# Kernel optimization log

Measured on AMD Instinct MI355X. Metric: run time of the kernel, lower is better.

Reference implementation:

```python
import jax, jax.numpy as jnp
import numpy as np
from jax import lax

N = 4096
IN_DIM, HID, OUT_DIM = 8, 64, 4
N_CONV = 10


def setup_inputs() -> dict:
    key = jax.random.key(0)
    ks = jax.random.split(key, 16)
    s = 0.05
    inp = {
        "inputs": jax.random.normal(ks[0], (N, IN_DIM), jnp.float32),
        "emb_w": jax.random.normal(ks[1], (IN_DIM, HID), jnp.float32) * s,
        "emb_b": jnp.zeros((HID,), jnp.float32),
        "q_w": jax.random.normal(ks[2], (HID, HID), jnp.float32) * s,
        "q_b": jnp.zeros((HID,), jnp.float32),
        "k_w": jax.random.normal(ks[3], (HID, HID), jnp.float32) * s,
        "k_b": jnp.zeros((HID,), jnp.float32),
        # 10 asymmetric conv layers: 1x3 kernel, 3x1 kernel, PReLU scalar (torch default 0.25)
        "conv_w1": jax.random.normal(ks[4], (N_CONV, 3), jnp.float32) * 0.3,
        "conv_w2": jax.random.normal(ks[5], (N_CONV, 3), jnp.float32) * 0.3,
        "conv_a": jnp.full((N_CONV,), 0.25, jnp.float32),
        "gcn_w": jax.random.normal(ks[6], (OUT_DIM, HID), jnp.float32) * s,
        "gcn_b": jnp.zeros((HID,), jnp.float32),
        "gcn_a": jnp.float32(0.25),
        "mlp_w1": jax.random.normal(ks[7], (HID, HID // 2), jnp.float32) * s,
        "mlp_b1": jnp.zeros((HID // 2,), jnp.float32),
        "mlp_w2": jax.random.normal(ks[8], (HID // 2, OUT_DIM), jnp.float32) * s,
        "mlp_b2": jnp.zeros((OUT_DIM,), jnp.float32),
    }
    return inp


def _asym_layer(x, w1, w2, a):
    # x: [1,1,N,N]; w1 -> 1x3 conv, w2 -> 3x1 conv, a -> PReLU scalar
    k1 = w1.reshape(1, 1, 1, 3)
    k2 = w2.reshape(1, 1, 3, 1)
    dn = ("NCHW", "OIHW", "NCHW")
    o = (lax.conv_general_dilated(x, k1, (1, 1), [(0, 0), (1, 1)], dimension_numbers=dn)
         + lax.conv_general_dilated(x, k2, (1, 1), [(1, 1), (0, 0)], dimension_numbers=dn))
    return jnp.where(o >= 0, o, a * o)


def reference(inputs, emb_w, emb_b, q_w, q_b, k_w, k_b,
              conv_w1, conv_w2, conv_a,
              gcn_w, gcn_b, gcn_a, mlp_w1, mlp_b1, mlp_w2, mlp_b2):
    o = inputs[:, 4:]                                   # [N, 4]
    x = inputs @ emb_w + emb_b                          # [N, H]
    q = x @ q_w + q_b                                   # [N, D]
    k = x @ k_w + k_b                                   # [N, D]
    scores = (q @ k.T) / jnp.sqrt(jnp.float32(k.shape[-1]))
    attn = jax.nn.softmax(scores, axis=-1)              # [N, N]

    h = attn[None, None]                                # [1,1,N,N]
    for i in range(N_CONV):
        h = _asym_layer(h, conv_w1[i], conv_w2[i], conv_a[i])
    conv_features = h[0, 0]                             # [N, N]

    mask = (jax.nn.sigmoid(conv_features) > 0.5).astype(attn.dtype)
    adjacency = mask * attn                             # [N, N]
    calc = adjacency @ o                                # [N, 4]

    g = calc @ gcn_w + gcn_b
    g = jnp.where(g >= 0, g, gcn_a * g)                 # PReLU
    m = jnp.maximum(g @ mlp_w1 + mlp_b1, 0.0)
    return m @ mlp_w2 + mlp_b2                          # [N, 4]
```

## Files before the change

### kernel.cpp

```cpp
#include <hip/hip_runtime.h>
#include <hip/hip_fp16.h>

#define NROWS 4096
#define HID 64

typedef _Float16 f16x8 __attribute__((ext_vector_type(8)));
typedef float f32x4 __attribute__((ext_vector_type(4)));

static __device__ __forceinline__ __half2 u2h(unsigned u) {
  __half2 h; __builtin_memcpy(&h, &u, 4); return h;
}
static __device__ __forceinline__ unsigned h2u(__half2 h) {
  unsigned u; __builtin_memcpy(&u, &h, 4); return u;
}

__global__ __launch_bounds__(64) void k_embed(
    const float* __restrict__ inp, const float* __restrict__ emb_w,
    const float* __restrict__ emb_b, const float* __restrict__ q_w,
    const float* __restrict__ q_b, const float* __restrict__ k_w,
    const float* __restrict__ k_b, __half* __restrict__ qh,
    __half* __restrict__ kh, float* __restrict__ opk) {
  int row = blockIdx.x;
  int t = threadIdx.x;
  __shared__ float in_s[8];
  __shared__ float x_s[64];
  if (t < 8) in_s[t] = inp[row * 8 + t];
  __syncthreads();
  float acc = emb_b[t];
#pragma unroll
  for (int i = 0; i < 8; ++i) acc += in_s[i] * emb_w[i * 64 + t];
  x_s[t] = acc;
  __syncthreads();
  float qa = q_b[t], ka = k_b[t];
#pragma unroll
  for (int i = 0; i < 64; ++i) {
    float xv = x_s[i];
    qa += xv * q_w[i * 64 + t];
    ka += xv * k_w[i * 64 + t];
  }
  qh[row * 64 + t] = __float2half(qa * 0.125f);
  kh[row * 64 + t] = __float2half(ka);
  if (t < 4) opk[row * 4 + t] = inp[row * 8 + 4 + t];
}

__global__ __launch_bounds__(512, 2) void k_scores(
    const __half* __restrict__ qh, const __half* __restrict__ kh,
    float* __restrict__ S) {
  __shared__ float redm[8][16];
  __shared__ float reds[8][16];
  int t = threadIdx.x;
  int w = t >> 6;
  int l = t & 63;
  int m16 = l & 15;
  int g4 = l >> 4;
  int rb = blockIdx.x * 16;
  const uint4* qq = (const uint4*)qh;
  const uint4* kk = (const uint4*)kh;
  int qrow = rb + m16;
  f16x8 a0 = __builtin_bit_cast(f16x8, qq[qrow * 8 + g4]);
  f16x8 a1 = __builtin_bit_cast(f16x8, qq[qrow * 8 + 4 + g4]);
  f32x4 acc[32];
#pragma unroll
  for (int i = 0; i < 32; ++i) acc[i] = (f32x4){0.f, 0.f, 0.f, 0.f};
#pragma unroll
  for (int i = 0; i < 32; ++i) {
    int kcol = (w * 32 + i) * 16 + m16;
    f16x8 b0 = __builtin_bit_cast(f16x8, kk[kcol * 8 + g4]);
    f16x8 b1 = __builtin_bit_cast(f16x8, kk[kcol * 8 + 4 + g4]);
    acc[i] = __builtin_amdgcn_mfma_f32_16x16x32_f16(a0, b0, acc[i], 0, 0, 0);
    acc[i] = __builtin_amdgcn_mfma_f32_16x16x32_f16(a1, b1, acc[i], 0, 0, 0);
  }
  float m4[4] = {-1e30f, -1e30f, -1e30f, -1e30f};
#pragma unroll
  for (int i = 0; i < 32; ++i) {
#pragma unroll
    for (int c = 0; c < 4; ++c) m4[c] = fmaxf(m4[c], acc[i][c]);
  }
#pragma unroll
  for (int off = 1; off < 16; off <<= 1) {
#pragma unroll
    for (int c = 0; c < 4; ++c) m4[c] = fmaxf(m4[c], __shfl_xor(m4[c], off, 64));
  }
  if (m16 == 0) {
#pragma unroll
    for (int c = 0; c < 4; ++c) redm[w][g4 * 4 + c] = m4[c];
  }
  __syncthreads();
#pragma unroll
  for (int c = 0; c < 4; ++c) {
    float mm = redm[0][g4 * 4 + c];
#pragma unroll
    for (int ww = 1; ww < 8; ++ww) mm = fmaxf(mm, redm[ww][g4 * 4 + c]);
    m4[c] = mm;
  }
  float s4[4] = {0.f, 0.f, 0.f, 0.f};
#pragma unroll
  for (int i = 0; i < 32; ++i) {
#pragma unroll
    for (int c = 0; c < 4; ++c) {
      float e = __expf(acc[i][c] - m4[c]);
      acc[i][c] = e;
      s4[c] += e;
    }
  }
#pragma unroll
  for (int off = 1; off < 16; off <<= 1) {
#pragma unroll
    for (int c = 0; c < 4; ++c) s4[c] += __shfl_xor(s4[c], off, 64);
  }
  if (m16 == 0) {
#pragma unroll
    for (int c = 0; c < 4; ++c) reds[w][g4 * 4 + c] = s4[c];
  }
  __syncthreads();
  float li[4];
#pragma unroll
  for (int c = 0; c < 4; ++c) {
    float ss = reds[0][g4 * 4 + c];
#pragma unroll
    for (int ww = 1; ww < 8; ++ww) ss += reds[ww][g4 * 4 + c];
    li[c] = 1.0f / ss;
  }
#pragma unroll
  for (int i = 0; i < 32; ++i) {
    int col = (w * 32 + i) * 16 + m16;
#pragma unroll
    for (int c = 0; c < 4; ++c) {
      S[(size_t)(rb + g4 * 4 + c) * NROWS + col] = acc[i][c] * li[c];
    }
  }
}

#define SWH 128
#define SHH 50
#define SSTRH 130
#define OWW 236
#define OHH 30
#define GX 18
#define GY 137

__global__ __launch_bounds__(512, 2) void k_conv3(
    const float* __restrict__ attn, float* __restrict__ partial,
    const float* __restrict__ w1p, const float* __restrict__ w2p,
    const float* __restrict__ ap, const float* __restrict__ opk) {
  __shared__ unsigned buf[2][SHH * SSTRH];
  int tid = threadIdx.x;
  int bx = blockIdx.x, by = blockIdx.y;
  int gi0 = by * OHH - 10;
  int gj0 = bx * OWW - 10;
  bool edge = (bx == 0) || (bx == GX - 1) || (by == 0) || (by == GY - 1);
  if (!edge) {
    for (int idx = tid; idx < SHH * SWH; idx += 512) {
      int r = idx >> 7, d = idx & 127;
      float2 v = *(const float2*)(attn + (size_t)(gi0 + r) * NROWS + gj0 + 2 * d);
      buf[0][r * SSTRH + d] =
          h2u(__float22half2_rn(make_float2(v.x * 256.f, v.y * 256.f)));
    }
  } else {
    for (int idx = tid; idx < SHH * SWH; idx += 512) {
      int r = idx >> 7, d = idx & 127;
      int gi = gi0 + r, gj = gj0 + 2 * d;
      float a = 0.f, b = 0.f;
      if ((unsigned)gi < (unsigned)NROWS) {
        if ((unsigned)gj < (unsigned)NROWS) a = attn[(size_t)gi * NROWS + gj] * 256.f;
        if ((unsigned)(gj + 1) < (unsigned)NROWS) b = attn[(size_t)gi * NROWS + gj + 1] * 256.f;
      }
      buf[0][r * SSTRH + d] = h2u(__float22half2_rn(make_float2(a, b)));
    }
  }
  __syncthreads();

  int wv = tid >> 6, l = tid & 63;
  int rb = 1 + 6 * wv;
  int doff = 2 * l;
  __half2 CM0 = __float2half2_rn(1.f), CM1 = __float2half2_rn(1.f);
  if (edge) {
    float m0 = ((unsigned)(gj0 + 4 * l + 0) < (unsigned)NROWS) ? 1.f : 0.f;
    float m1 = ((unsigned)(gj0 + 4 * l + 1) < (unsigned)NROWS) ? 1.f : 0.f;
    float m2 = ((unsigned)(gj0 + 4 * l + 2) < (unsigned)NROWS) ? 1.f : 0.f;
    float m3 = ((unsigned)(gj0 + 4 * l + 3) < (unsigned)NROWS) ? 1.f : 0.f;
    CM0 = __float22half2_rn(make_float2(m0, m1));
    CM1 = __float22half2_rn(make_float2(m2, m3));
  }

  for (int p = 0; p < 10; ++p) {
    unsigned* src = buf[p & 1];
    unsigned* dst = buf[(p + 1) & 1];
    __half2 W10 = __float2half2_rn(w1p[3 * p]);
    __half2 W12 = __float2half2_rn(w1p[3 * p + 2]);
    __half2 WC  = __float2half2_rn(w1p[3 * p + 1] + w2p[3 * p + 1]);
    __half2 W20 = __float2half2_rn(w2p[3 * p]);
    __half2 W22 = __float2half2_rn(w2p[3 * p + 2]);
    __half2 AL  = __float2half2_rn(ap[p]);
    uint2 Vm = *(uint2*)&src[(rb - 1) * SSTRH + doff];
    uint2 Vc = *(uint2*)&src[rb * SSTRH + doff];
#pragma unroll
    for (int s = 0; s < 6; ++s) {
      int r = rb + s;
      uint2 Vp = *(uint2*)&src[(r + 1) * SSTRH + doff];
      unsigned Lm1 = (unsigned)__builtin_amdgcn_update_dpp(
          0, (int)Vc.y, 0x138, 0xF, 0xF, true);
      unsigned Hp1 = (unsigned)__builtin_amdgcn_update_dpp(
          0, (int)Vc.x, 0x130, 0xF, 0xF, true);
      unsigned SL0 = __builtin_amdgcn_alignbit(Vc.x, Lm1, 16);
      unsigned SR0 = __builtin_amdgcn_alignbit(Vc.y, Vc.x, 16);
      unsigned SR1 = __builtin_amdgcn_alignbit(Hp1, Vc.y, 16);
      __half2 o0 = __hmul2(WC, u2h(Vc.x));
      o0 = __hfma2(W10, u2h(SL0), o0);
      o0 = __hfma2(W12, u2h(SR0), o0);
      o0 = __hfma2(W20, u2h(Vm.x), o0);
      o0 = __hfma2(W22, u2h(Vp.x), o0);
      __half2 o1 = __hmul2(WC, u2h(Vc.y));
      o1 = __hfma2(W10, u2h(SR0), o1);
      o1 = __hfma2(W12, u2h(SR1), o1);
      o1 = __hfma2(W20, u2h(Vm.y), o1);
      o1 = __hfma2(W22, u2h(Vp.y), o1);
      {
        unsigned u0 = h2u(o0), ua0 = h2u(__hmul2(AL, o0)), r0;
        asm("v_pk_max_f16 %0, %1, %2" : "=v"(r0) : "v"(u0), "v"(ua0));
        o0 = u2h(r0);
        unsigned u1 = h2u(o1), ua1 = h2u(__hmul2(AL, o1)), r1;
        asm("v_pk_max_f16 %0, %1, %2" : "=v"(r1) : "v"(u1), "v"(ua1));
        o1 = u2h(r1);
      }
      if (edge) {
        o0 = __hmul2(o0, CM0);
        o1 = __hmul2(o1, CM1);
        if ((unsigned)(gi0 + r) >= (unsigned)NROWS) {
          o0 = __float2half2_rn(0.f);
          o1 = __float2half2_rn(0.f);
        }
      }
      uint2 res = {h2u(o0), h2u(o1)};
      *(uint2*)&dst[r * SSTRH + doff] = res;
      Vm = Vc; Vc = Vp;
    }
    __syncthreads();
  }

  const unsigned* fin = buf[0];
  int i = tid >> 4;
  int part = tid & 15;
  int gi = gi0 + 10 + i;
  float a0 = 0.f, a1 = 0.f, a2 = 0.f, a3 = 0.f;
  if (i < OHH && gi < NROWS) {
    for (int g = part; g < 59; g += 16) {
      int jc = 10 + 4 * g;
      int gj = gj0 + jc;
      if (gj + 3 < NROWS) {
        unsigned d0 = fin[(10 + i) * SSTRH + (jc >> 1)];
        unsigned d1 = fin[(10 + i) * SSTRH + (jc >> 1) + 1];
        __half2 h0 = u2h(d0), h1 = u2h(d1);
        float4 av = *(const float4*)(attn + (size_t)gi * NROWS + gj);
        const float4* op = (const float4*)opk;
        if (__low2float(h0) > 0.f)  { float4 o = op[gj + 0]; a0 += av.x * o.x; a1 += av.x * o.y; a2 += av.x * o.z; a3 += av.x * o.w; }
        if (__high2float(h0) > 0.f) { float4 o = op[gj + 1]; a0 += av.y * o.x; a1 += av.y * o.y; a2 += av.y * o.z; a3 += av.y * o.w; }
        if (__low2float(h1) > 0.f)  { float4 o = op[gj + 2]; a0 += av.z * o.x; a1 += av.z * o.y; a2 += av.z * o.z; a3 += av.z * o.w; }
        if (__high2float(h1) > 0.f) { float4 o = op[gj + 3]; a0 += av.w * o.x; a1 += av.w * o.y; a2 += av.w * o.z; a3 += av.w * o.w; }
      }
    }
  }
#pragma unroll
  for (int off = 1; off < 16; off <<= 1) {
    a0 += __shfl_xor(a0, off, 64);
    a1 += __shfl_xor(a1, off, 64);
    a2 += __shfl_xor(a2, off, 64);
    a3 += __shfl_xor(a3, off, 64);
  }
  if (part == 0 && i < OHH && gi < NROWS) {
    float4 r = {a0, a1, a2, a3};
    *(float4*)&partial[((size_t)bx * NROWS + gi) * 4] = r;
  }
}

__global__ __launch_bounds__(64) void k_head(
    const float* __restrict__ partial, const float* __restrict__ gcn_w,
    const float* __restrict__ gcn_b, const float* __restrict__ gcn_a,
    const float* __restrict__ w1, const float* __restrict__ b1,
    const float* __restrict__ w2, const float* __restrict__ b2,
    float* __restrict__ out) {
  int row = blockIdx.x;
  int t = threadIdx.x;
  __shared__ float c4[4];
  __shared__ float gs[64];
  __shared__ float ms[32];
  {
    int c = t & 3, gg = t >> 2;
    float s = partial[((size_t)gg * NROWS + row) * 4 + c];
    if (gg < GX - 16)
      s += partial[((size_t)(gg + 16) * NROWS + row) * 4 + c];
#pragma unroll
    for (int off = 4; off < 64; off <<= 1) s += __shfl_xor(s, off, 64);
    if (t < 4) c4[t] = s;
  }
  __syncthreads();
  float g = gcn_b[t];
#pragma unroll
  for (int d = 0; d < 4; ++d) g += c4[d] * gcn_w[d * 64 + t];
  float ga = gcn_a[0];
  gs[t] = (g >= 0.f) ? g : ga * g;
  __syncthreads();
  if (t < 32) {
    float mm = b1[t];
#pragma unroll
    for (int i = 0; i < 64; ++i) mm += gs[i] * w1[i * 32 + t];
    ms[t] = fmaxf(mm, 0.f);
  }
  __syncthreads();
  if (t < 4) {
    float o = b2[t];
#pragma unroll
    for (int i = 0; i < 32; ++i) o += ms[i] * w2[i * 4 + t];
    out[row * 4 + t] = o;
  }
}

extern "C" void kernel_launch(void* const* d_in, const int* in_sizes, int n_in,
                              void* d_out, int out_size, void* d_ws, size_t ws_size,
                              hipStream_t stream) {
  (void)in_sizes; (void)n_in; (void)out_size; (void)ws_size;
  const float* inp    = (const float*)d_in[0];
  const float* emb_w  = (const float*)d_in[1];
  const float* emb_b  = (const float*)d_in[2];
  const float* q_w    = (const float*)d_in[3];
  const float* q_b    = (const float*)d_in[4];
  const float* k_w    = (const float*)d_in[5];
  const float* k_b    = (const float*)d_in[6];
  const float* conv_w1 = (const float*)d_in[7];
  const float* conv_w2 = (const float*)d_in[8];
  const float* conv_a  = (const float*)d_in[9];
  const float* gcn_w  = (const float*)d_in[10];
  const float* gcn_b  = (const float*)d_in[11];
  const float* gcn_a  = (const float*)d_in[12];
  const float* mlp_w1 = (const float*)d_in[13];
  const float* mlp_b1 = (const float*)d_in[14];
  const float* mlp_w2 = (const float*)d_in[15];
  const float* mlp_b2 = (const float*)d_in[16];
  float* out = (float*)d_out;

  const size_t NN = (size_t)NROWS * NROWS;
  float* A       = (float*)d_ws;
  float* partial = A + NN;
  float* qhf     = partial + (size_t)GX * NROWS * 4;
  float* khf     = qhf + (size_t)NROWS * HID / 2;
  float* opk     = khf + (size_t)NROWS * HID / 2;

  k_embed<<<NROWS, 64, 0, stream>>>(inp, emb_w, emb_b, q_w, q_b, k_w, k_b,
                                    (__half*)qhf, (__half*)khf, opk);
  k_scores<<<NROWS / 16, 512, 0, stream>>>((const __half*)qhf,
                                           (const __half*)khf, A);
  k_conv3<<<dim3(GX, GY), 512, 0, stream>>>(A, partial, conv_w1, conv_w2,
                                            conv_a, opk);
  k_head<<<NROWS, 64, 0, stream>>>(partial, gcn_w, gcn_b, gcn_a, mlp_w1, mlp_b1,
                                   mlp_w2, mlp_b2, out);
}
```

Baseline: 129.0 us.

## Use larger single-buffered conv tiles with 4 half2 per lane in-place update

The fused 10-layer stencil kernel now uses a single LDS buffer updated in place instead of ping-pong buffers. Each wave handles 7 rows, keeping the first and last rows in registers until after a barrier so neighbouring waves still read old values. Tiles grow to 512 columns by 58 rows, cutting the 10-cell halo recompute overhead and the grid count (9x108). Each lane now processes 8 columns via uint4 loads, which raises register pressure and adds a second barrier per layer.

```diff
diff --git a/kernel.cpp b/kernel.cpp
--- a/kernel.cpp
+++ b/kernel.cpp
@@ -131,90 +131,101 @@
   }
 }
 
-#define SWH 128
-#define SHH 50
-#define SSTRH 130
-#define OWW 236
-#define OHH 30
-#define GX 18
-#define GY 137
-
-__global__ __launch_bounds__(512, 2) void k_conv3(
+#define CSD 256
+#define CSH 58
+#define COW 492
+#define COH 38
+#define CGX 9
+#define CGY 108
+
+__global__ __launch_bounds__(512, 2) void k_conv4(
     const float* __restrict__ attn, float* __restrict__ partial,
     const float* __restrict__ w1p, const float* __restrict__ w2p,
     const float* __restrict__ ap, const float* __restrict__ opk) {
-  __shared__ unsigned buf[2][SHH * SSTRH];
+  __shared__ unsigned buf[CSH * CSD];
   int tid = threadIdx.x;
   int bx = blockIdx.x, by = blockIdx.y;
-  int gi0 = by * OHH - 10;
-  int gj0 = bx * OWW - 10;
-  bool edge = (bx == 0) || (bx == GX - 1) || (by == 0) || (by == GY - 1);
+  int gi0 = by * COH - 10;
+  int gj0 = bx * COW - 10;
+  bool edge = (bx == 0) || (bx == CGX - 1) || (by == 0) || (by == CGY - 1);
   if (!edge) {
-    for (int idx = tid; idx < SHH * SWH; idx += 512) {
-      int r = idx >> 7, d = idx & 127;
+    for (int idx = tid; idx < CSH * CSD; idx += 512) {
+      int r = idx >> 8, d = idx & 255;
       float2 v = *(const float2*)(attn + (size_t)(gi0 + r) * NROWS + gj0 + 2 * d);
-      buf[0][r * SSTRH + d] =
-          h2u(__float22half2_rn(make_float2(v.x * 256.f, v.y * 256.f)));
+      buf[idx] = h2u(__float22half2_rn(make_float2(v.x * 256.f, v.y * 256.f)));
     }
   } else {
-    for (int idx = tid; idx < SHH * SWH; idx += 512) {
-      int r = idx >> 7, d = idx & 127;
+    for (int idx = tid; idx < CSH * CSD; idx += 512) {
+      int r = idx >> 8, d = idx & 255;
       int gi = gi0 + r, gj = gj0 + 2 * d;
       float a = 0.f, b = 0.f;
       if ((unsigned)gi < (unsigned)NROWS) {
         if ((unsigned)gj < (unsigned)NROWS) a = attn[(size_t)gi * NROWS + gj] * 256.f;
         if ((unsigned)(gj + 1) < (unsigned)NROWS) b = attn[(size_t)gi * NROWS + gj + 1] * 256.f;
       }
-      buf[0][r * SSTRH + d] = h2u(__float22half2_rn(make_float2(a, b)));
+      buf[idx] = h2u(__float22half2_rn(make_float2(a, b)));
     }
   }
   __syncthreads();
 
   int wv = tid >> 6, l = tid & 63;
-  int rb = 1 + 6 * wv;
-  int doff = 2 * l;
-  __half2 CM0 = __float2half2_rn(1.f), CM1 = __float2half2_rn(1.f);
+  int rb = 1 + 7 * wv;
+  int doff = 4 * l;
+  __half2 CM[4];
+#pragma unroll
+  for (int d = 0; d < 4; ++d) CM[d] = __float2half2_rn(1.f);
   if (edge) {
-    float m0 = ((unsigned)(gj0 + 4 * l + 0) < (unsigned)NROWS) ? 1.f : 0.f;
-    float m1 = ((unsigned)(gj0 + 4 * l + 1) < (unsigned)NROWS) ? 1.f : 0.f;
-    float m2 = ((unsigned)(gj0 + 4 * l + 2) < (unsigned)NROWS) ? 1.f : 0.f;
-    float m3 = ((unsigned)(gj0 + 4 * l + 3) < (unsigned)NROWS) ? 1.f : 0.f;
-    CM0 = __float22half2_rn(make_float2(m0, m1));
-    CM1 = __float22half2_rn(make_float2(m2, m3));
+#pragma unroll
+    for (int d = 0; d < 4; ++d) {
+      float mlo = ((unsigned)(gj0 + 8 * l + 2 * d) < (unsigned)NROWS) ? 1.f : 0.f;
+      float mhi = ((unsigned)(gj0 + 8 * l + 2 * d + 1) < (unsigned)NROWS) ? 1.f : 0.f;
+      CM[d] = __float22half2_rn(make_float2(mlo, mhi));
+    }
   }
 
   for (int p = 0; p < 10; ++p) {
-    unsigned* src = buf[p & 1];
-    unsigned* dst = buf[(p + 1) & 1];
     __half2 W10 = __float2half2_rn(w1p[3 * p]);
     __half2 W12 = __float2half2_rn(w1p[3 * p + 2]);
     __half2 WC  = __float2half2_rn(w1p[3 * p + 1] + w2p[3 * p + 1]);
     __half2 W20 = __float2half2_rn(w2p[3 * p]);
     __half2 W22 = __float2half2_rn(w2p[3 * p + 2]);
     __half2 AL  = __float2half2_rn(ap[p]);
-    uint2 Vm = *(uint2*)&src[(rb - 1) * SSTRH + doff];
-    uint2 Vc = *(uint2*)&src[rb * SSTRH + doff];
-#pragma unroll
-    for (int s = 0; s < 6; ++s) {
+    uint4 Vm = *(uint4*)&buf[(rb - 1) * CSD + doff];
+    uint4 Vc = *(uint4*)&buf[rb * CSD + doff];
+    uint4 dfirst, dlast;
+#pragma unroll
+    for (int s = 0; s < 7; ++s) {
       int r = rb + s;
-      uint2 Vp = *(uint2*)&src[(r + 1) * SSTRH + doff];
+      uint4 Vp = *(uint4*)&buf[(r + 1) * CSD + doff];
       unsigned Lm1 = (unsigned)__builtin_amdgcn_update_dpp(
-          0, (int)Vc.y, 0x138, 0xF, 0xF, true);
+          0, (int)Vc.w, 0x138, 0xF, 0xF, true);
       unsigned Hp1 = (unsigned)__builtin_amdgcn_update_dpp(
           0, (int)Vc.x, 0x130, 0xF, 0xF, true);
-      unsigned SL0 = __builtin_amdgcn_alignbit(Vc.x, Lm1, 16);
-      unsigned SR0 = __builtin_amdgcn_alignbit(Vc.y, Vc.x, 16);
-      unsigned SR1 = __builtin_amdgcn_alignbit(Hp1, Vc.y, 16);
+      unsigned A0 = __builtin_amdgcn_alignbit(Vc.x, Lm1, 16);
+      unsigned A1 = __builtin_amdgcn_alignbit(Vc.y, Vc.x, 16);
+      unsigned A2 = __builtin_amdgcn_alignbit(Vc.z, Vc.y, 16);
+      unsigned A3 = __builtin_amdgcn_alignbit(Vc.w, Vc.z, 16);
+      unsigned A4 = __builtin_amdgcn_alignbit(Hp1, Vc.w, 16);
       __half2 o0 = __hmul2(WC, u2h(Vc.x));
-      o0 = __hfma2(W10, u2h(SL0), o0);
-      o0 = __hfma2(W12, u2h(SR0), o0);
+      o0 = __hfma2(W10, u2h(A0), o0);
+      o0 = __hfma2(W12, u2h(A1), o0);
       o0 = __hfma2(W20, u2h(Vm.x), o0);
       o0 = __hfma2(W22, u2h(Vp.x), o0);
       __half2 o1 = __hmul2(WC, u2h(Vc.y));
-      o1 = __hfma2(W10, u2h(SR0), o1);
-      o1 = __hfma2(W12, u2h(SR1), o1);
+      o1 = __hfma2(W10, u2h(A1), o1);
+      o1 = __hfma2(W12, u2h(A2), o1);
       o1 = __hfma2(W20, u2h(Vm.y), o1);
       o1 = __hfma2(W22, u2h(Vp.y), o1);
+      __half2 o2 = __hmul2(WC, u2h(Vc.z));
+      o2 = __hfma2(W10, u2h(A2), o2);
+      o2 = __hfma2(W12, u2h(A3), o2);
+      o2 = __hfma2(W20, u2h(Vm.z), o2);
+      o2 = __hfma2(W22, u2h(Vp.z), o2);
+      __half2 o3 = __hmul2(WC, u2h(Vc.w));
+      o3 = __hfma2(W10, u2h(A3), o3);
+      o3 = __hfma2(W12, u2h(A4), o3);
+      o3 = __hfma2(W20, u2h(Vm.w), o3);
+      o3 = __hfma2(W22, u2h(Vp.w), o3);
       {
         unsigned u0 = h2u(o0), ua0 = h2u(__hmul2(AL, o0)), r0;
         asm("v_pk_max_f16 %0, %1, %2" : "=v"(r0) : "v"(u0), "v"(ua0));
@@ -222,37 +233,50 @@
         unsigned u1 = h2u(o1), ua1 = h2u(__hmul2(AL, o1)), r1;
         asm("v_pk_max_f16 %0, %1, %2" : "=v"(r1) : "v"(u1), "v"(ua1));
         o1 = u2h(r1);
+        unsigned u2 = h2u(o2), ua2 = h2u(__hmul2(AL, o2)), r2;
+        asm("v_pk_max_f16 %0, %1, %2" : "=v"(r2) : "v"(u2), "v"(ua2));
+        o2 = u2h(r2);
+        unsigned u3 = h2u(o3), ua3 = h2u(__hmul2(AL, o3)), r3;
+        asm("v_pk_max_f16 %0, %1, %2" : "=v"(r3) : "v"(u3), "v"(ua3));
+        o3 = u2h(r3);
       }
       if (edge) {
-        o0 = __hmul2(o0, CM0);
-        o1 = __hmul2(o1, CM1);
+        o0 = __hmul2(o0, CM[0]);
+        o1 = __hmul2(o1, CM[1]);
+        o2 = __hmul2(o2, CM[2]);
+        o3 = __hmul2(o3, CM[3]);
         if ((unsigned)(gi0 + r) >= (unsigned)NROWS) {
-          o0 = __float2half2_rn(0.f);
-          o1 = __float2half2_rn(0.f);
+          o0 = __float2half2_rn(0.f); o1 = __float2half2_rn(0.f);
+          o2 = __float2half2_rn(0.f); o3 = __float2half2_rn(0.f);
         }
       }
-      uint2 res = {h2u(o0), h2u(o1)};
-      *(uint2*)&dst[r * SSTRH + doff] = res;
+      uint4 res = {h2u(o0), h2u(o1), h2u(o2), h2u(o3)};
+      if (s == 0) dfirst = res;
+      else if (s == 6) dlast = res;
+      else *(uint4*)&buf[r * CSD + doff] = res;
       Vm = Vc; Vc = Vp;
     }
     __syncthreads();
-  }
-
-  const unsigned* fin = buf[0];
-  int i = tid >> 4;
-  int part = tid & 15;
+    *(uint4*)&buf[rb * CSD + doff] = dfirst;
+    *(uint4*)&buf[(rb + 6) * CSD + doff] = dlast;
+    __syncthreads();
+  }
+
+  const unsigned* fin = buf;
+  int i = tid >> 3;
+  int part = tid & 7;
   int gi = gi0 + 10 + i;
   float a0 = 0.f, a1 = 0.f, a2 = 0.f, a3 = 0.f;
-  if (i < OHH && gi < NROWS) {
-    for (int g = part; g < 59; g += 16) {
+  if (i < COH && gi < NROWS) {
+    const float4* op = (const float4*)opk;
+    for (int g = part; g < 123; g += 8) {
       int jc = 10 + 4 * g;
       int gj = gj0 + jc;
       if (gj + 3 < NROWS) {
-        unsigned d0 = fin[(10 + i) * SSTRH + (jc >> 1)];
-        unsigned d1 = fin[(10 + i) * SSTRH + (jc >> 1) + 1];
+        unsigned d0 = fin[(10 + i) * CSD + (jc >> 1)];
+        unsigned d1 = fin[(10 + i) * CSD + (jc >> 1) + 1];
         __half2 h0 = u2h(d0), h1 = u2h(d1);
         float4 av = *(const float4*)(attn + (size_t)gi * NROWS + gj);
-        const float4* op = (const float4*)opk;
         if (__low2float(h0) > 0.f)  { float4 o = op[gj + 0]; a0 += av.x * o.x; a1 += av.x * o.y; a2 += av.x * o.z; a3 += av.x * o.w; }
         if (__high2float(h0) > 0.f) { float4 o = op[gj + 1]; a0 += av.y * o.x; a1 += av.y * o.y; a2 += av.y * o.z; a3 += av.y * o.w; }
         if (__low2float(h1) > 0.f)  { float4 o = op[gj + 2]; a0 += av.z * o.x; a1 += av.z * o.y; a2 += av.z * o.z; a3 += av.z * o.w; }
@@ -261,13 +285,13 @@
     }
   }
 #pragma unroll
-  for (int off = 1; off < 16; off <<= 1) {
+  for (int off = 1; off < 8; off <<= 1) {
     a0 += __shfl_xor(a0, off, 64);
     a1 += __shfl_xor(a1, off, 64);
     a2 += __shfl_xor(a2, off, 64);
     a3 += __shfl_xor(a3, off, 64);
   }
-  if (part == 0 && i < OHH && gi < NROWS) {
+  if (part == 0 && i < COH && gi < NROWS) {
     float4 r = {a0, a1, a2, a3};
     *(float4*)&partial[((size_t)bx * NROWS + gi) * 4] = r;
   }
@@ -286,9 +310,8 @@
   __shared__ float ms[32];
   {
     int c = t & 3, gg = t >> 2;
-    float s = partial[((size_t)gg * NROWS + row) * 4 + c];
-    if (gg < GX - 16)
-      s += partial[((size_t)(gg + 16) * NROWS + row) * 4 + c];
+    float s = 0.f;
+    if (gg < CGX) s = partial[((size_t)gg * NROWS + row) * 4 + c];
 #pragma unroll
     for (int off = 4; off < 64; off <<= 1) s += __shfl_xor(s, off, 64);
     if (t < 4) c4[t] = s;
@@ -341,7 +364,7 @@
   const size_t NN = (size_t)NROWS * NROWS;
   float* A       = (float*)d_ws;
   float* partial = A + NN;
-  float* qhf     = partial + (size_t)GX * NROWS * 4;
+  float* qhf     = partial + (size_t)18 * NROWS * 4;
   float* khf     = qhf + (size_t)NROWS * HID / 2;
   float* opk     = khf + (size_t)NROWS * HID / 2;
 
@@ -349,8 +372,8 @@
                                     (__half*)qhf, (__half*)khf, opk);
   k_scores<<<NROWS / 16, 512, 0, stream>>>((const __half*)qhf,
                                            (const __half*)khf, A);
-  k_conv3<<<dim3(GX, GY), 512, 0, stream>>>(A, partial, conv_w1, conv_w2,
-                                            conv_a, opk);
+  k_conv4<<<dim3(CGX, CGY), 512, 0, stream>>>(A, partial, conv_w1, conv_w2,
+                                              conv_a, opk);
   k_head<<<NROWS, 64, 0, stream>>>(partial, gcn_w, gcn_b, gcn_a, mlp_w1, mlp_b1,
                                    mlp_w2, mlp_b2, out);
 }
```

New measurement: 148.5 us. 15.1% more time.

## Use in-place single LDS buffer for conv stencil to enlarge tiles and cut halo

Applied to the files above, without the earlier changes.

The 10-layer fused stencil kernel now updates a single shared-memory tile in place. Each wave holds its first and last output rows in registers and writes them back after a barrier. The LDS saved goes to taller tiles (46 output rows instead of 30), which lowers the fraction of halo rows recomputed and the number of blocks. The cost is an extra barrier per layer and a different split of the final masked reduction across threads.

```diff
diff --git a/kernel.cpp b/kernel.cpp
--- a/kernel.cpp
+++ b/kernel.cpp
@@ -131,33 +131,32 @@
   }
 }
 
-#define SWH 128
-#define SHH 50
-#define SSTRH 130
-#define OWW 236
-#define OHH 30
-#define GX 18
-#define GY 137
-
-__global__ __launch_bounds__(512, 2) void k_conv3(
+#define C5D 130
+#define C5H 66
+#define C5OW 236
+#define C5OH 46
+#define C5GX 18
+#define C5GY 90
+
+__global__ __launch_bounds__(512, 2) void k_conv5(
     const float* __restrict__ attn, float* __restrict__ partial,
     const float* __restrict__ w1p, const float* __restrict__ w2p,
     const float* __restrict__ ap, const float* __restrict__ opk) {
-  __shared__ unsigned buf[2][SHH * SSTRH];
+  __shared__ unsigned buf[C5H * C5D];
   int tid = threadIdx.x;
   int bx = blockIdx.x, by = blockIdx.y;
-  int gi0 = by * OHH - 10;
-  int gj0 = bx * OWW - 10;
-  bool edge = (bx == 0) || (bx == GX - 1) || (by == 0) || (by == GY - 1);
+  int gi0 = by * C5OH - 10;
+  int gj0 = bx * C5OW - 10;
+  bool edge = (bx == 0) || (bx == C5GX - 1) || (by == 0) || (by == C5GY - 1);
   if (!edge) {
-    for (int idx = tid; idx < SHH * SWH; idx += 512) {
+    for (int idx = tid; idx < C5H * 128; idx += 512) {
       int r = idx >> 7, d = idx & 127;
       float2 v = *(const float2*)(attn + (size_t)(gi0 + r) * NROWS + gj0 + 2 * d);
-      buf[0][r * SSTRH + d] =
+      buf[r * C5D + d] =
           h2u(__float22half2_rn(make_float2(v.x * 256.f, v.y * 256.f)));
     }
   } else {
-    for (int idx = tid; idx < SHH * SWH; idx += 512) {
+    for (int idx = tid; idx < C5H * 128; idx += 512) {
       int r = idx >> 7, d = idx & 127;
       int gi = gi0 + r, gj = gj0 + 2 * d;
       float a = 0.f, b = 0.f;
@@ -165,13 +164,13 @@
         if ((unsigned)gj < (unsigned)NROWS) a = attn[(size_t)gi * NROWS + gj] * 256.f;
         if ((unsigned)(gj + 1) < (unsigned)NROWS) b = attn[(size_t)gi * NROWS + gj + 1] * 256.f;
       }
-      buf[0][r * SSTRH + d] = h2u(__float22half2_rn(make_float2(a, b)));
+      buf[r * C5D + d] = h2u(__float22half2_rn(make_float2(a, b)));
     }
   }
   __syncthreads();
 
   int wv = tid >> 6, l = tid & 63;
-  int rb = 1 + 6 * wv;
+  int rb = 1 + 8 * wv;
   int doff = 2 * l;
   __half2 CM0 = __float2half2_rn(1.f), CM1 = __float2half2_rn(1.f);
   if (edge) {
@@ -184,20 +183,19 @@
   }
 
   for (int p = 0; p < 10; ++p) {
-    unsigned* src = buf[p & 1];
-    unsigned* dst = buf[(p + 1) & 1];
     __half2 W10 = __float2half2_rn(w1p[3 * p]);
     __half2 W12 = __float2half2_rn(w1p[3 * p + 2]);
     __half2 WC  = __float2half2_rn(w1p[3 * p + 1] + w2p[3 * p + 1]);
     __half2 W20 = __float2half2_rn(w2p[3 * p]);
     __half2 W22 = __float2half2_rn(w2p[3 * p + 2]);
     __half2 AL  = __float2half2_rn(ap[p]);
-    uint2 Vm = *(uint2*)&src[(rb - 1) * SSTRH + doff];
-    uint2 Vc = *(uint2*)&src[rb * SSTRH + doff];
-#pragma unroll
-    for (int s = 0; s < 6; ++s) {
+    uint2 Vm = *(uint2*)&buf[(rb - 1) * C5D + doff];
+    uint2 Vc = *(uint2*)&buf[rb * C5D + doff];
+    uint2 dfirst, dlast;
+#pragma unroll
+    for (int s = 0; s < 8; ++s) {
       int r = rb + s;
-      uint2 Vp = *(uint2*)&src[(r + 1) * SSTRH + doff];
+      uint2 Vp = *(uint2*)&buf[(r + 1) * C5D + doff];
       unsigned Lm1 = (unsigned)__builtin_amdgcn_update_dpp(
           0, (int)Vc.y, 0x138, 0xF, 0xF, true);
       unsigned Hp1 = (unsigned)__builtin_amdgcn_update_dpp(
@@ -232,27 +230,32 @@
         }
       }
       uint2 res = {h2u(o0), h2u(o1)};
-      *(uint2*)&dst[r * SSTRH + doff] = res;
+      if (s == 0) dfirst = res;
+      else if (s == 7) dlast = res;
+      else *(uint2*)&buf[r * C5D + doff] = res;
       Vm = Vc; Vc = Vp;
     }
     __syncthreads();
-  }
-
-  const unsigned* fin = buf[0];
-  int i = tid >> 4;
-  int part = tid & 15;
+    *(uint2*)&buf[rb * C5D + doff] = dfirst;
+    *(uint2*)&buf[(rb + 7) * C5D + doff] = dlast;
+    __syncthreads();
+  }
+
+  const unsigned* fin = buf;
+  int i = tid >> 3;
+  int part = tid & 7;
   int gi = gi0 + 10 + i;
   float a0 = 0.f, a1 = 0.f, a2 = 0.f, a3 = 0.f;
-  if (i < OHH && gi < NROWS) {
-    for (int g = part; g < 59; g += 16) {
+  if (i < C5OH && gi < NROWS) {
+    const float4* op = (const float4*)opk;
+    for (int g = part; g < 59; g += 8) {
       int jc = 10 + 4 * g;
       int gj = gj0 + jc;
       if (gj + 3 < NROWS) {
-        unsigned d0 = fin[(10 + i) * SSTRH + (jc >> 1)];
-        unsigned d1 = fin[(10 + i) * SSTRH + (jc >> 1) + 1];
+        unsigned d0 = fin[(10 + i) * C5D + (jc >> 1)];
+        unsigned d1 = fin[(10 + i) * C5D + (jc >> 1) + 1];
         __half2 h0 = u2h(d0), h1 = u2h(d1);
         float4 av = *(const float4*)(attn + (size_t)gi * NROWS + gj);
-        const float4* op = (const float4*)opk;
         if (__low2float(h0) > 0.f)  { float4 o = op[gj + 0]; a0 += av.x * o.x; a1 += av.x * o.y; a2 += av.x * o.z; a3 += av.x * o.w; }
         if (__high2float(h0) > 0.f) { float4 o = op[gj + 1]; a0 += av.y * o.x; a1 += av.y * o.y; a2 += av.y * o.z; a3 += av.y * o.w; }
         if (__low2float(h1) > 0.f)  { float4 o = op[gj + 2]; a0 += av.z * o.x; a1 += av.z * o.y; a2 += av.z * o.z; a3 += av.z * o.w; }
@@ -261,13 +264,13 @@
     }
   }
 #pragma unroll
-  for (int off = 1; off < 16; off <<= 1) {
+  for (int off = 1; off < 8; off <<= 1) {
     a0 += __shfl_xor(a0, off, 64);
     a1 += __shfl_xor(a1, off, 64);
     a2 += __shfl_xor(a2, off, 64);
     a3 += __shfl_xor(a3, off, 64);
   }
-  if (part == 0 && i < OHH && gi < NROWS) {
+  if (part == 0 && i < C5OH && gi < NROWS) {
     float4 r = {a0, a1, a2, a3};
     *(float4*)&partial[((size_t)bx * NROWS + gi) * 4] = r;
   }
@@ -287,7 +290,7 @@
   {
     int c = t & 3, gg = t >> 2;
     float s = partial[((size_t)gg * NROWS + row) * 4 + c];
-    if (gg < GX - 16)
+    if (gg < C5GX - 16)
       s += partial[((size_t)(gg + 16) * NROWS + row) * 4 + c];
 #pragma unroll
     for (int off = 4; off < 64; off <<= 1) s += __shfl_xor(s, off, 64);
@@ -341,7 +344,7 @@
   const size_t NN = (size_t)NROWS * NROWS;
   float* A       = (float*)d_ws;
   float* partial = A + NN;
-  float* qhf     = partial + (size_t)GX * NROWS * 4;
+  float* qhf     = partial + (size_t)18 * NROWS * 4;
   float* khf     = qhf + (size_t)NROWS * HID / 2;
   float* opk     = khf + (size_t)NROWS * HID / 2;
 
@@ -349,8 +352,8 @@
                                     (__half*)qhf, (__half*)khf, opk);
   k_scores<<<NROWS / 16, 512, 0, stream>>>((const __half*)qhf,
                                            (const __half*)khf, A);
-  k_conv3<<<dim3(GX, GY), 512, 0, stream>>>(A, partial, conv_w1, conv_w2,
-                                            conv_a, opk);
+  k_conv5<<<dim3(C5GX, C5GY), 512, 0, stream>>>(A, partial, conv_w1, conv_w2,
+                                                conv_a, opk);
   k_head<<<NROWS, 64, 0, stream>>>(partial, gcn_w, gcn_b, gcn_a, mlp_w1, mlp_b1,
                                    mlp_w2, mlp_b2, out);
 }
```

Measured after the change: 120.0 us. 7.0% less time.
